# Optimization experiments

Measured on AMD Instinct MI355X. Metric: run time of the kernel, lower is better.

Reference implementation:

```python
import jax, jax.numpy as jnp
import numpy as np

N = 200000   # nodes
E = 600000   # directed edges
G = 8192     # graphs in batch
D_IN = 30
H = 128


def setup_inputs() -> dict:
    key = jax.random.key(0)
    ks = jax.random.split(key, 9)
    x = jax.random.normal(ks[0], (N, D_IN), jnp.float32)
    edge_index = jax.random.randint(ks[1], (2, E), 0, N, dtype=jnp.int32)
    batch_idx = jnp.sort(jax.random.randint(ks[2], (N,), 0, G, dtype=jnp.int32))
    W1 = jax.random.normal(ks[3], (D_IN, H), jnp.float32) / np.sqrt(D_IN)
    b1 = jnp.zeros((H,), jnp.float32)
    W2 = jax.random.normal(ks[4], (H, H), jnp.float32) / np.sqrt(H)
    b2 = jnp.zeros((H,), jnp.float32)
    W3 = jax.random.normal(ks[5], (H, H), jnp.float32) / np.sqrt(H)
    b3 = jnp.zeros((H,), jnp.float32)
    return {"x": x, "edge_index": edge_index, "batch_idx": batch_idx,
            "W1": W1, "b1": b1, "W2": W2, "b2": b2, "W3": W3, "b3": b3}


def _gcn_layer(x, W, b, src, dst, dinv):
    h = x @ W                                   # [N, H]
    norm = (dinv[src] * dinv[dst])[:, None]     # per-edge normalization
    msg = h[src] * norm                         # [E, H] gather + scale
    agg = jax.ops.segment_sum(msg, dst, num_segments=N)
    agg = agg + h * (dinv * dinv)[:, None]      # self-loop term, norm = 1/deg
    return jax.nn.relu(agg + b)


def reference(x, edge_index, batch_idx, W1, b1, W2, b2, W3, b3):
    src, dst = edge_index[0], edge_index[1]
    # degree with self-loops (edge weight 1), aggregated at target (col)
    deg = 1.0 + jax.ops.segment_sum(jnp.ones((E,), x.dtype), dst, num_segments=N)
    dinv = jax.lax.rsqrt(deg)                   # deg >= 1, safe
    h = _gcn_layer(x, W1, b1, src, dst, dinv)
    h = _gcn_layer(h, W2, b2, src, dst, dinv)
    h = _gcn_layer(h, W3, b3, src, dst, dinv)
    # global mean pool over batch segments
    sums = jax.ops.segment_sum(h, batch_idx, num_segments=G)
    counts = jax.ops.segment_sum(jnp.ones((N,), h.dtype), batch_idx, num_segments=G)
    return sums / jnp.maximum(counts, 1.0)[:, None]
```

## Files before the change

kernel.cpp:

```cpp
#include <hip/hip_runtime.h>


#define DIN 30
#define HD  128

typedef __attribute__((ext_vector_type(8))) short v8s;
typedef __attribute__((ext_vector_type(4))) float v4f;

static __device__ __forceinline__ unsigned short f2bf(float f) {
  unsigned int u = __float_as_uint(f);
  u += 0x7fffu + ((u >> 16) & 1u);
  return (unsigned short)(u >> 16);
}
static __device__ __forceinline__ float bf2f(unsigned short s) {
  return __uint_as_float(((unsigned int)s) << 16);
}
static __device__ __forceinline__ float bflo(unsigned int u) {
  return __uint_as_float(u << 16);
}
static __device__ __forceinline__ float bfhi(unsigned int u) {
  return __uint_as_float(u & 0xffff0000u);
}

#define ACC8(v, s)                                            \
  {                                                           \
    a0 += (s) * (float)((v).x & 0xffu);                       \
    a1 += (s) * (float)(((v).x >> 8) & 0xffu);                \
    a2 += (s) * (float)(((v).x >> 16) & 0xffu);               \
    a3 += (s) * (float)((v).x >> 24);                         \
    a4 += (s) * (float)((v).y & 0xffu);                       \
    a5 += (s) * (float)(((v).y >> 8) & 0xffu);                \
    a6 += (s) * (float)(((v).y >> 16) & 0xffu);               \
    a7 += (s) * (float)((v).y >> 24);                         \
  }

__global__ void k_degree(const int* __restrict__ dst, int* __restrict__ deg,
                         int* __restrict__ eord, int E) {
  int e = blockIdx.x * blockDim.x + threadIdx.x;
  if (e < E) eord[e] = atomicAdd(&deg[dst[e]], 1);
}

__global__ void k_scan(const int* __restrict__ deg, int* __restrict__ scanbuf,
                       int* __restrict__ rowptr, float* __restrict__ dinv, int N) {
  __shared__ int s[256];
  __shared__ int sbase;
  int bid = blockIdx.x, tid = threadIdx.x;
  int base = bid * 1024 + tid * 4;
  int v[4]; int t = 0;
#pragma unroll
  for (int j = 0; j < 4; ++j) { int idx = base + j; v[j] = (idx < N) ? deg[idx] : 0; t += v[j]; }
  s[tid] = t; __syncthreads();
  for (int d = 1; d < 256; d <<= 1) {
    int u = (tid >= d) ? s[tid - d] : 0;
    __syncthreads();
    s[tid] += u;
    __syncthreads();
  }
  int myexcl = s[tid] - t;
  int blocktotal = s[255];
  if (tid == 0) atomicExch(&scanbuf[bid], blocktotal | 0x80000000);

  int pre = 0;
  for (int p = tid; p < bid; p += 256) {
    int val;
    do { val = atomicAdd(&scanbuf[p], 0); } while (!(val & 0x80000000));
    pre += val & 0x7fffffff;
  }
  __syncthreads();
  s[tid] = pre; __syncthreads();
  for (int d = 128; d > 0; d >>= 1) { if (tid < d) s[tid] += s[tid + d]; __syncthreads(); }
  if (tid == 0) sbase = s[0];
  __syncthreads();

  int run = sbase + myexcl;
#pragma unroll
  for (int j = 0; j < 4; ++j) {
    int idx = base + j;
    if (idx < N) {
      rowptr[idx] = run;
      dinv[idx] = rsqrtf((float)(1 + v[j]));
    }
    run += v[j];
    if (idx == N - 1) rowptr[N] = run;
  }
}

static __device__ __forceinline__ void wtf_one(const float* __restrict__ W,
                                               unsigned short* __restrict__ WTF,
                                               int idx, int Kreal, int KK) {
  int j = idx & 7;
  int c = idx >> 3;
  int l15 = c & 15;
  int quad = (c >> 4) & 3;
  int kk = (c >> 6) % KK;
  int t = c / (64 * KK);
  int k = kk * 32 + quad * 8 + j;
  int n = t * 16 + l15;
  WTF[idx] = (k < Kreal) ? f2bf(W[k * 128 + n]) : (unsigned short)0;
}

__global__ void k_prep(const int* __restrict__ src, const int* __restrict__ dst,
                       const int* __restrict__ rowptr, const int* __restrict__ eord,
                       int* __restrict__ col, int E,
                       const float* __restrict__ x, const float* __restrict__ dinv,
                       unsigned short* __restrict__ xb, int N,
                       const float* __restrict__ W1, const float* __restrict__ W2,
                       const float* __restrict__ W3,
                       unsigned short* __restrict__ W1F, unsigned short* __restrict__ W2F,
                       unsigned short* __restrict__ W3F,
                       const int* __restrict__ batch, int* __restrict__ gstart, int G,
                       float* __restrict__ out,
                       int SB, int XB, int WB, int BB) {
  int blk = blockIdx.x;
  if (blk < SB) {
    int e = blk * 256 + threadIdx.x;
    if (e < E) col[rowptr[dst[e]] + eord[e]] = src[e];
  } else if (blk < SB + XB) {
    int idx = (blk - SB) * 256 + threadIdx.x;
    if (idx < N * 32) {
      int n = idx >> 5, f = idx & 31;
      float v = (f < DIN) ? x[(size_t)n * DIN + f] * dinv[n] : 0.f;
      xb[idx] = f2bf(v);
    }
  } else if (blk < SB + XB + WB) {
    int idx = (blk - SB - XB) * 256 + threadIdx.x;
    if (idx < 4096) wtf_one(W1, W1F, idx, DIN, 1);
    else if (idx < 20480) wtf_one(W2, W2F, idx - 4096, 128, 4);
    else if (idx < 36864) wtf_one(W3, W3F, idx - 20480, 128, 4);
  } else if (blk < SB + XB + WB + BB) {
    int i = (blk - SB - XB - WB) * 256 + threadIdx.x;
    if (i >= N) return;
    int b = batch[i];
    int prev = (i == 0) ? -1 : batch[i - 1];
    for (int g = prev + 1; g <= b; ++g) gstart[g] = i;
    if (i == N - 1)
      for (int g = b + 1; g <= G; ++g) gstart[g] = N;
  } else {
    int idx = (blk - SB - XB - WB - BB) * 256 + threadIdx.x;
    if (idx < G * 32)
      ((float4*)out)[idx] = make_float4(0.f, 0.f, 0.f, 0.f);
  }
}

template <int K>
__global__ __launch_bounds__(1024, 8) void k_fused(const void* __restrict__ hin,
                                                   const float* __restrict__ hscale,
                                                   const unsigned short* __restrict__ WTF,
                                                   const float* __restrict__ b,
                                                   const int* __restrict__ rowptr,
                                                   const int* __restrict__ col,
                                                   const float* __restrict__ dinv,
                                                   unsigned char* __restrict__ Cq,
                                                   float* __restrict__ Cs, int N) {
  constexpr int KK = K / 32;
  constexpr int KP = (K == 128) ? 136 : 40;
  constexpr int CP = 132;
  constexpr int SMSZ = (64 * KP > 64 * CP) ? 64 * KP : 64 * CP;
  constexpr int CH = 256;
  constexpr int SST = (K == 128) ? 144 : 72;
  __shared__ __align__(16) unsigned short sm[SMSZ];
  __shared__ __align__(16) unsigned char stg[CH * SST];
  __shared__ float sscale[(K == 128) ? CH : 1];

  int tid = threadIdx.x;
  int l16 = tid & 15;
  int g = tid >> 4;
  int row0 = blockIdx.x * 64;
  int node = row0 + g;
  int rend = row0 + 64; if (rend > N) rend = N;

  float a0 = 0.f, a1 = 0.f, a2 = 0.f, a3 = 0.f, a4 = 0.f, a5 = 0.f, a6 = 0.f, a7 = 0.f;
  int e0 = 0, e1 = 0; float di = 0.f;
  if (node < N) {
    e0 = rowptr[node]; e1 = rowptr[node + 1]; di = dinv[node];
    if constexpr (K == 32) {
      unsigned int u = ((const unsigned int*)hin)[(size_t)node * 16 + l16];
      a0 = bflo(u); a1 = bfhi(u);
    } else {
      uint2 u = ((const uint2*)hin)[(size_t)node * 16 + l16];
      float s = hscale[node];
      ACC8(u, s);
    }
  }
  int eb = rowptr[row0];
  int ee = rowptr[rend];

  for (int c0 = eb; c0 < ee; c0 += CH) {
#pragma unroll
    for (int q = 0; q < (CH * 8) / 1024; ++q) {
      int slot = q * 1024 + tid;
      int eL = slot >> 3, l8 = slot & 7;
      int e = c0 + eL;
      if (e < ee) {
        int c = col[e];
        if constexpr (K == 32) {
          uint2 v = ((const uint2*)hin)[(size_t)c * 8 + l8];
          *(uint2*)&stg[eL * SST + l8 * 8] = v;
        } else {
          uint4 v = ((const uint4*)hin)[(size_t)c * 8 + l8];
          *(uint4*)&stg[eL * SST + l8 * 16] = v;
          if (l8 == 0) sscale[eL] = hscale[c];
        }
      }
    }
    __syncthreads();
    int lo = (e0 > c0) ? e0 : c0;
    int hi = (e1 < c0 + CH) ? e1 : (c0 + CH);
    int e2 = lo;
    for (; e2 + 2 <= hi; e2 += 2) {
      int i0 = e2 - c0, i1 = i0 + 1;
      if constexpr (K == 32) {
        unsigned int w0 = *(const unsigned int*)&stg[i0 * SST + l16 * 4];
        unsigned int w1 = *(const unsigned int*)&stg[i1 * SST + l16 * 4];
        a0 += bflo(w0); a1 += bfhi(w0);
        a0 += bflo(w1); a1 += bfhi(w1);
      } else {
        uint2 w0 = *(const uint2*)&stg[i0 * SST + l16 * 8];
        uint2 w1 = *(const uint2*)&stg[i1 * SST + l16 * 8];
        float s0 = sscale[i0], s1 = sscale[i1];
        ACC8(w0, s0);
        ACC8(w1, s1);
      }
    }
    if (e2 < hi) {
      int i0 = e2 - c0;
      if constexpr (K == 32) {
        unsigned int w0 = *(const unsigned int*)&stg[i0 * SST + l16 * 4];
        a0 += bflo(w0); a1 += bfhi(w0);
      } else {
        uint2 w0 = *(const uint2*)&stg[i0 * SST + l16 * 8];
        float s0 = sscale[i0];
        ACC8(w0, s0);
      }
    }
    __syncthreads();
  }

  if constexpr (K == 32) {
    *(unsigned int*)&sm[g * KP + l16 * 2] =
        (unsigned int)f2bf(a0 * di) | ((unsigned int)f2bf(a1 * di) << 16);
  } else {
    uint4 o;
    o.x = (unsigned int)f2bf(a0 * di) | ((unsigned int)f2bf(a1 * di) << 16);
    o.y = (unsigned int)f2bf(a2 * di) | ((unsigned int)f2bf(a3 * di) << 16);
    o.z = (unsigned int)f2bf(a4 * di) | ((unsigned int)f2bf(a5 * di) << 16);
    o.w = (unsigned int)f2bf(a6 * di) | ((unsigned int)f2bf(a7 * di) << 16);
    *(uint4*)&sm[g * KP + l16 * 8] = o;
  }
  __syncthreads();

  int wv = tid >> 6, lane = tid & 63, quad = lane >> 4, l15 = lane & 15;
  int rt = wv & 3, tp = wv >> 2;
  v8s af[KK];
#pragma unroll
  for (int kk = 0; kk < KK; ++kk)
    af[kk] = *(const v8s*)&sm[(rt * 16 + l15) * KP + kk * 32 + quad * 8];
  __syncthreads();

  int crow0 = row0 + rt * 16 + quad * 4;
  float dr[4];
  if (crow0 + 3 < N) {
    float4 d4 = *(const float4*)&dinv[crow0];
    dr[0] = d4.x; dr[1] = d4.y; dr[2] = d4.z; dr[3] = d4.w;
  } else {
#pragma unroll
    for (int i = 0; i < 4; ++i) dr[i] = (crow0 + i < N) ? dinv[crow0 + i] : 0.f;
  }

#pragma unroll
  for (int tt = 0; tt < 2; ++tt) {
    int t = tp * 2 + tt;
    v4f acc = {0.f, 0.f, 0.f, 0.f};
#pragma unroll
    for (int kk = 0; kk < KK; ++kk) {
      v8s bf = *(const v8s*)(WTF + (size_t)(((t * KK + kk) * 4 + quad) * 16 + l15) * 8);
      acc = __builtin_amdgcn_mfma_f32_16x16x32_bf16(af[kk], bf, acc, 0, 0, 0);
    }
    float bias = b[t * 16 + l15];
#pragma unroll
    for (int i = 0; i < 4; ++i) {
      float o = fmaxf(acc[i] + bias, 0.f) * dr[i];
      sm[(rt * 16 + quad * 4 + i) * CP + t * 16 + l15] = f2bf(o);
    }
  }
  __syncthreads();

  {
    uint4 u = *(const uint4*)&sm[g * CP + l16 * 8];
    float f0 = bflo(u.x), f1 = bfhi(u.x), f2 = bflo(u.y), f3 = bfhi(u.y);
    float f4 = bflo(u.z), f5 = bfhi(u.z), f6 = bflo(u.w), f7 = bfhi(u.w);
    float m = fmaxf(fmaxf(fmaxf(f0, f1), fmaxf(f2, f3)),
                    fmaxf(fmaxf(f4, f5), fmaxf(f6, f7)));
    m = fmaxf(m, __shfl_xor(m, 1));
    m = fmaxf(m, __shfl_xor(m, 2));
    m = fmaxf(m, __shfl_xor(m, 4));
    m = fmaxf(m, __shfl_xor(m, 8));
    float inv = (m > 0.f) ? 255.f / m : 0.f;
    unsigned q0 = (unsigned)__float2int_rn(fminf(f0 * inv, 255.f));
    unsigned q1 = (unsigned)__float2int_rn(fminf(f1 * inv, 255.f));
    unsigned q2 = (unsigned)__float2int_rn(fminf(f2 * inv, 255.f));
    unsigned q3 = (unsigned)__float2int_rn(fminf(f3 * inv, 255.f));
    unsigned q4 = (unsigned)__float2int_rn(fminf(f4 * inv, 255.f));
    unsigned q5 = (unsigned)__float2int_rn(fminf(f5 * inv, 255.f));
    unsigned q6 = (unsigned)__float2int_rn(fminf(f6 * inv, 255.f));
    unsigned q7 = (unsigned)__float2int_rn(fminf(f7 * inv, 255.f));
    uint2 o;
    o.x = q0 | (q1 << 8) | (q2 << 16) | (q3 << 24);
    o.y = q4 | (q5 << 8) | (q6 << 16) | (q7 << 24);
    int row = row0 + g;
    if (row < N) {
      ((uint2*)Cq)[(size_t)row * 16 + l16] = o;
      if (l16 == 0) Cs[row] = m * (1.f / 255.f);
    }
  }
}

__global__ __launch_bounds__(1024, 8) void k_fused_pool(const unsigned char* __restrict__ hin,
                                                        const float* __restrict__ hscale,
                                                        const unsigned short* __restrict__ WTF,
                                                        const float* __restrict__ b,
                                                        const int* __restrict__ rowptr,
                                                        const int* __restrict__ col,
                                                        const float* __restrict__ dinv,
                                                        const int* __restrict__ batch,
                                                        float* __restrict__ out, int N) {
  constexpr int KK = 4, KP = 136, CP = 132;
  constexpr int SMSZ = 64 * KP;
  constexpr int CH = 256, SST = 144;
  __shared__ __align__(16) unsigned short sm[SMSZ];
  __shared__ __align__(16) unsigned char stg[CH * SST];
  __shared__ float sscale[CH];
  __shared__ int sbatch[64];

  int tid = threadIdx.x;
  int l16 = tid & 15;
  int g = tid >> 4;
  int row0 = blockIdx.x * 64;
  int node = row0 + g;
  int rend = row0 + 64; if (rend > N) rend = N;

  if (tid < 64) sbatch[tid] = (row0 + tid < N) ? batch[row0 + tid] : -1;

  float a0 = 0.f, a1 = 0.f, a2 = 0.f, a3 = 0.f, a4 = 0.f, a5 = 0.f, a6 = 0.f, a7 = 0.f;
  int e0 = 0, e1 = 0; float di = 0.f;
  if (node < N) {
    e0 = rowptr[node]; e1 = rowptr[node + 1]; di = dinv[node];
    uint2 u = ((const uint2*)hin)[(size_t)node * 16 + l16];
    float s = hscale[node];
    ACC8(u, s);
  }
  int eb = rowptr[row0];
  int ee = rowptr[rend];

  for (int c0 = eb; c0 < ee; c0 += CH) {
#pragma unroll
    for (int q = 0; q < 2; ++q) {
      int slot = q * 1024 + tid;
      int eL = slot >> 3, l8 = slot & 7;
      int e = c0 + eL;
      if (e < ee) {
        int c = col[e];
        uint4 v = ((const uint4*)hin)[(size_t)c * 8 + l8];
        *(uint4*)&stg[eL * SST + l8 * 16] = v;
        if (l8 == 0) sscale[eL] = hscale[c];
      }
    }
    __syncthreads();
    int lo = (e0 > c0) ? e0 : c0;
    int hi = (e1 < c0 + CH) ? e1 : (c0 + CH);
    int e2 = lo;
    for (; e2 + 2 <= hi; e2 += 2) {
      int i0 = e2 - c0, i1 = i0 + 1;
      uint2 w0 = *(const uint2*)&stg[i0 * SST + l16 * 8];
      uint2 w1 = *(const uint2*)&stg[i1 * SST + l16 * 8];
      float s0 = sscale[i0], s1 = sscale[i1];
      ACC8(w0, s0);
      ACC8(w1, s1);
    }
    if (e2 < hi) {
      int i0 = e2 - c0;
      uint2 w0 = *(const uint2*)&stg[i0 * SST + l16 * 8];
      float s0 = sscale[i0];
      ACC8(w0, s0);
    }
    __syncthreads();
  }

  {
    uint4 o;
    o.x = (unsigned int)f2bf(a0 * di) | ((unsigned int)f2bf(a1 * di) << 16);
    o.y = (unsigned int)f2bf(a2 * di) | ((unsigned int)f2bf(a3 * di) << 16);
    o.z = (unsigned int)f2bf(a4 * di) | ((unsigned int)f2bf(a5 * di) << 16);
    o.w = (unsigned int)f2bf(a6 * di) | ((unsigned int)f2bf(a7 * di) << 16);
    *(uint4*)&sm[g * KP + l16 * 8] = o;
  }
  __syncthreads();

  int wv = tid >> 6, lane = tid & 63, quad = lane >> 4, l15 = lane & 15;
  int rt = wv & 3, tp = wv >> 2;
  v8s af[KK];
#pragma unroll
  for (int kk = 0; kk < KK; ++kk)
    af[kk] = *(const v8s*)&sm[(rt * 16 + l15) * KP + kk * 32 + quad * 8];
  __syncthreads();

#pragma unroll
  for (int tt = 0; tt < 2; ++tt) {
    int t = tp * 2 + tt;
    v4f acc = {0.f, 0.f, 0.f, 0.f};
#pragma unroll
    for (int kk = 0; kk < KK; ++kk) {
      v8s bf = *(const v8s*)(WTF + (size_t)(((t * KK + kk) * 4 + quad) * 16 + l15) * 8);
      acc = __builtin_amdgcn_mfma_f32_16x16x32_bf16(af[kk], bf, acc, 0, 0, 0);
    }
    float bias = b[t * 16 + l15];
#pragma unroll
    for (int i = 0; i < 4; ++i) {
      float o = fmaxf(acc[i] + bias, 0.f);
      sm[(rt * 16 + quad * 4 + i) * CP + t * 16 + l15] = f2bf(o);
    }
  }
  __syncthreads();

  int f = tid & 127;
  int grp = tid >> 7;
  float run = 0.f;
  int cur = -1;
#pragma unroll
  for (int j = 0; j < 8; ++j) {
    int r = grp * 8 + j;
    int gg = sbatch[r];
    if (gg != cur) {
      if (cur >= 0) atomicAdd(&out[(size_t)cur * 128 + f], run);
      run = 0.f; cur = gg;
    }
    if (gg >= 0) run += bf2f(sm[r * CP + f]);
  }
  if (cur >= 0) atomicAdd(&out[(size_t)cur * 128 + f], run);
}

__global__ void k_finalize(float* __restrict__ out, const int* __restrict__ gstart, int G) {
  int idx = blockIdx.x * blockDim.x + threadIdx.x;
  if (idx >= G * 128) return;
  int g = idx >> 7;
  float cnt = (float)(gstart[g + 1] - gstart[g]);
  out[idx] = out[idx] / fmaxf(cnt, 1.f);
}

extern "C" void kernel_launch(void* const* d_in, const int* in_sizes, int n_in,
                              void* d_out, int out_size, void* d_ws, size_t ws_size,
                              hipStream_t stream) {
  const float* x  = (const float*)d_in[0];
  const int* ei   = (const int*)d_in[1];
  const int* batch = (const int*)d_in[2];
  const float* W1 = (const float*)d_in[3];
  const float* b1 = (const float*)d_in[4];
  const float* W2 = (const float*)d_in[5];
  const float* b2 = (const float*)d_in[6];
  const float* W3 = (const float*)d_in[7];
  const float* b3 = (const float*)d_in[8];
  float* out = (float*)d_out;
  int N = in_sizes[2];
  int E = in_sizes[1] / 2;
  int G = out_size / HD;
  const int* src = ei;
  const int* dst = ei + E;

  size_t off = 0;
  char* ws = (char*)d_ws;
  auto alloc = [&](size_t bytes) -> void* {
    void* p = ws + off;
    off += (bytes + 255) & ~(size_t)255;
    return p;
  };
  int nb1024 = (N + 1023) / 1024;
  int*   deg     = (int*)alloc((size_t)N * 4);
  int*   scanbuf = (int*)alloc((size_t)nb1024 * 4);
  float* dinv    = (float*)alloc((size_t)N * 4);
  int*   rowptr  = (int*)alloc((size_t)(N + 1) * 4);
  int*   eord    = (int*)alloc((size_t)E * 4);
  int*   col     = (int*)alloc((size_t)E * 4);
  int*   gstart  = (int*)alloc((size_t)(G + 1) * 4);
  unsigned short* xb  = (unsigned short*)alloc((size_t)N * 32 * 2);
  unsigned char*  hAq = (unsigned char*)alloc((size_t)N * 128);
  float*          hAs = (float*)alloc((size_t)N * 4);
  unsigned char*  hBq = (unsigned char*)alloc((size_t)N * 128);
  float*          hBs = (float*)alloc((size_t)N * 4);
  unsigned short* W1F = (unsigned short*)alloc(4096 * 2);
  unsigned short* W2F = (unsigned short*)alloc(16384 * 2);
  unsigned short* W3F = (unsigned short*)alloc(16384 * 2);
  (void)ws_size; (void)n_in;

  size_t zbytes = (size_t)((char*)dinv - (char*)deg);
  hipMemsetAsync(deg, 0, zbytes, stream);
  k_degree<<<(E + 255) / 256, 256, 0, stream>>>(dst, deg, eord, E);
  k_scan<<<nb1024, 256, 0, stream>>>(deg, scanbuf, rowptr, dinv, N);

  int SB = (E + 255) / 256;
  int XB = (N * 32 + 255) / 256;
  int WB = 144;
  int BB = (N + 255) / 256;
  int ZB = (G * 32 + 255) / 256;
  k_prep<<<SB + XB + WB + BB + ZB, 256, 0, stream>>>(src, dst, rowptr, eord, col, E,
                                                     x, dinv, xb, N,
                                                     W1, W2, W3, W1F, W2F, W3F,
                                                     batch, gstart, G, out,
                                                     SB, XB, WB, BB);

  int fusedBlocks = (N + 63) / 64;
  k_fused<32><<<fusedBlocks, 1024, 0, stream>>>(xb, nullptr, W1F, b1, rowptr, col, dinv,
                                                hAq, hAs, N);
  k_fused<128><<<fusedBlocks, 1024, 0, stream>>>(hAq, hAs, W2F, b2, rowptr, col, dinv,
                                                 hBq, hBs, N);
  k_fused_pool<<<fusedBlocks, 1024, 0, stream>>>(hBq, hBs, W3F, b3, rowptr, col, dinv,
                                                 batch, out, N);
  k_finalize<<<(G * 128 + 255) / 256, 256, 0, stream>>>(out, gstart, G);
}
```

Baseline: 286.0 us.

## Materialize per-edge messages via source-sorted gather before each fused layer

Builds a source-sorted edge list with a permutation into destination order, then adds a separate gather kernel per layer that reads node features in source order and scatters them into a dense per-edge message buffer laid out in destination (CSR) order. The fused aggregation kernels then stream contiguous messages instead of doing random indexed reads through col. The aim is more coalesced, cache-friendly feature reads. The cost is an extra E x 128-byte buffer written and read per layer, a second degree count, a second scan, and extra kernel launches.

New measurement: 371.3 us. 29.8% more time.

```diff
diff --git a/kernel.cpp b/kernel.cpp
--- a/kernel.cpp
+++ b/kernel.cpp
@@ -34,21 +34,25 @@
     a7 += (s) * (float)((v).y >> 24);                         \
   }
 
-__global__ void k_degree(const int* __restrict__ dst, int* __restrict__ deg,
-                         int* __restrict__ eord, int E) {
+__global__ void k_degree2(const int* __restrict__ src, const int* __restrict__ dst,
+                          int* __restrict__ deg, int* __restrict__ sdeg,
+                          int* __restrict__ eord, int* __restrict__ seord, int E) {
   int e = blockIdx.x * blockDim.x + threadIdx.x;
-  if (e < E) eord[e] = atomicAdd(&deg[dst[e]], 1);
-}
-
-__global__ void k_scan(const int* __restrict__ deg, int* __restrict__ scanbuf,
-                       int* __restrict__ rowptr, float* __restrict__ dinv, int N) {
+  if (e < E) {
+    eord[e] = atomicAdd(&deg[dst[e]], 1);
+    seord[e] = atomicAdd(&sdeg[src[e]], 1);
+  }
+}
+
+__global__ void k_scan(const int* __restrict__ cnt, int* __restrict__ scanbuf,
+                       int* __restrict__ outptr, float* __restrict__ dinvp, int N) {
   __shared__ int s[256];
   __shared__ int sbase;
   int bid = blockIdx.x, tid = threadIdx.x;
   int base = bid * 1024 + tid * 4;
   int v[4]; int t = 0;
 #pragma unroll
-  for (int j = 0; j < 4; ++j) { int idx = base + j; v[j] = (idx < N) ? deg[idx] : 0; t += v[j]; }
+  for (int j = 0; j < 4; ++j) { int idx = base + j; v[j] = (idx < N) ? cnt[idx] : 0; t += v[j]; }
   s[tid] = t; __syncthreads();
   for (int d = 1; d < 256; d <<= 1) {
     int u = (tid >= d) ? s[tid - d] : 0;
@@ -77,11 +81,11 @@
   for (int j = 0; j < 4; ++j) {
     int idx = base + j;
     if (idx < N) {
-      rowptr[idx] = run;
-      dinv[idx] = rsqrtf((float)(1 + v[j]));
+      outptr[idx] = run;
+      if (dinvp) dinvp[idx] = rsqrtf((float)(1 + v[j]));
     }
     run += v[j];
-    if (idx == N - 1) rowptr[N] = run;
+    if (idx == N - 1) outptr[N] = run;
   }
 }
 
@@ -100,8 +104,9 @@
 }
 
 __global__ void k_prep(const int* __restrict__ src, const int* __restrict__ dst,
-                       const int* __restrict__ rowptr, const int* __restrict__ eord,
-                       int* __restrict__ col, int E,
+                       const int* __restrict__ rowptr, const int* __restrict__ srowptr,
+                       const int* __restrict__ eord, const int* __restrict__ seord,
+                       int* __restrict__ ssrc, int* __restrict__ sperm, int E,
                        const float* __restrict__ x, const float* __restrict__ dinv,
                        unsigned short* __restrict__ xb, int N,
                        const float* __restrict__ W1, const float* __restrict__ W2,
@@ -114,7 +119,13 @@
   int blk = blockIdx.x;
   if (blk < SB) {
     int e = blk * 256 + threadIdx.x;
-    if (e < E) col[rowptr[dst[e]] + eord[e]] = src[e];
+    if (e < E) {
+      int d = dst[e], s = src[e];
+      int pos_d = rowptr[d] + eord[e];
+      int pos_s = srowptr[s] + seord[e];
+      ssrc[pos_s] = s;
+      sperm[pos_s] = pos_d;
+    }
   } else if (blk < SB + XB) {
     int idx = (blk - SB) * 256 + threadIdx.x;
     if (idx < N * 32) {
@@ -142,13 +153,32 @@
   }
 }
 
+template <int RB>
+__global__ void k_gather(const void* __restrict__ hin, const float* __restrict__ hs,
+                         const int* __restrict__ ssrc, const int* __restrict__ sperm,
+                         void* __restrict__ msg, float* __restrict__ mscale, int E) {
+  constexpr int L = RB / 16;
+  int idx = blockIdx.x * blockDim.x + threadIdx.x;
+  int e = idx / L;
+  int l = idx & (L - 1);
+  if (e >= E) return;
+  int s = ssrc[e];
+  int p = sperm[e];
+  uint4 v = ((const uint4*)hin)[(size_t)s * L + l];
+  ((uint4*)msg)[(size_t)p * L + l] = v;
+  if constexpr (RB == 128) {
+    if (l == 0) mscale[p] = hs[s];
+  }
+}
+
 template <int K>
 __global__ __launch_bounds__(1024, 8) void k_fused(const void* __restrict__ hin,
                                                    const float* __restrict__ hscale,
+                                                   const void* __restrict__ msg,
+                                                   const float* __restrict__ mscale,
                                                    const unsigned short* __restrict__ WTF,
                                                    const float* __restrict__ b,
                                                    const int* __restrict__ rowptr,
-                                                   const int* __restrict__ col,
                                                    const float* __restrict__ dinv,
                                                    unsigned char* __restrict__ Cq,
                                                    float* __restrict__ Cs, int N) {
@@ -187,19 +217,18 @@
 
   for (int c0 = eb; c0 < ee; c0 += CH) {
 #pragma unroll
-    for (int q = 0; q < (CH * 8) / 1024; ++q) {
+    for (int q = 0; q < 2; ++q) {
       int slot = q * 1024 + tid;
       int eL = slot >> 3, l8 = slot & 7;
       int e = c0 + eL;
       if (e < ee) {
-        int c = col[e];
         if constexpr (K == 32) {
-          uint2 v = ((const uint2*)hin)[(size_t)c * 8 + l8];
+          uint2 v = ((const uint2*)msg)[(size_t)e * 8 + l8];
           *(uint2*)&stg[eL * SST + l8 * 8] = v;
         } else {
-          uint4 v = ((const uint4*)hin)[(size_t)c * 8 + l8];
+          uint4 v = ((const uint4*)msg)[(size_t)e * 8 + l8];
           *(uint4*)&stg[eL * SST + l8 * 16] = v;
-          if (l8 == 0) sscale[eL] = hscale[c];
+          if (l8 == 0) sscale[eL] = mscale[e];
         }
       }
     }
@@ -317,10 +346,11 @@
 
 __global__ __launch_bounds__(1024, 8) void k_fused_pool(const unsigned char* __restrict__ hin,
                                                         const float* __restrict__ hscale,
+                                                        const void* __restrict__ msg,
+                                                        const float* __restrict__ mscale,
                                                         const unsigned short* __restrict__ WTF,
                                                         const float* __restrict__ b,
                                                         const int* __restrict__ rowptr,
-                                                        const int* __restrict__ col,
                                                         const float* __restrict__ dinv,
                                                         const int* __restrict__ batch,
                                                         float* __restrict__ out, int N) {
@@ -359,10 +389,9 @@
       int eL = slot >> 3, l8 = slot & 7;
       int e = c0 + eL;
       if (e < ee) {
-        int c = col[e];
-        uint4 v = ((const uint4*)hin)[(size_t)c * 8 + l8];
+        uint4 v = ((const uint4*)msg)[(size_t)e * 8 + l8];
         *(uint4*)&stg[eL * SST + l8 * 16] = v;
-        if (l8 == 0) sscale[eL] = hscale[c];
+        if (l8 == 0) sscale[eL] = mscale[e];
       }
     }
     __syncthreads();
@@ -474,18 +503,25 @@
     return p;
   };
   int nb1024 = (N + 1023) / 1024;
-  int*   deg     = (int*)alloc((size_t)N * 4);
-  int*   scanbuf = (int*)alloc((size_t)nb1024 * 4);
+  int*   deg      = (int*)alloc((size_t)N * 4);
+  int*   sdeg     = (int*)alloc((size_t)N * 4);
+  int*   scanbuf  = (int*)alloc((size_t)nb1024 * 4);
+  int*   scanbuf2 = (int*)alloc((size_t)nb1024 * 4);
   float* dinv    = (float*)alloc((size_t)N * 4);
   int*   rowptr  = (int*)alloc((size_t)(N + 1) * 4);
+  int*   srowptr = (int*)alloc((size_t)(N + 1) * 4);
   int*   eord    = (int*)alloc((size_t)E * 4);
-  int*   col     = (int*)alloc((size_t)E * 4);
+  int*   seord   = (int*)alloc((size_t)E * 4);
+  int*   ssrc    = (int*)alloc((size_t)E * 4);
+  int*   sperm   = (int*)alloc((size_t)E * 4);
   int*   gstart  = (int*)alloc((size_t)(G + 1) * 4);
   unsigned short* xb  = (unsigned short*)alloc((size_t)N * 32 * 2);
   unsigned char*  hAq = (unsigned char*)alloc((size_t)N * 128);
   float*          hAs = (float*)alloc((size_t)N * 4);
   unsigned char*  hBq = (unsigned char*)alloc((size_t)N * 128);
   float*          hBs = (float*)alloc((size_t)N * 4);
+  unsigned char*  msg = (unsigned char*)alloc((size_t)E * 128);
+  float*          mscale = (float*)alloc((size_t)E * 4);
   unsigned short* W1F = (unsigned short*)alloc(4096 * 2);
   unsigned short* W2F = (unsigned short*)alloc(16384 * 2);
   unsigned short* W3F = (unsigned short*)alloc(16384 * 2);
@@ -493,26 +529,34 @@
 
   size_t zbytes = (size_t)((char*)dinv - (char*)deg);
   hipMemsetAsync(deg, 0, zbytes, stream);
-  k_degree<<<(E + 255) / 256, 256, 0, stream>>>(dst, deg, eord, E);
+  k_degree2<<<(E + 255) / 256, 256, 0, stream>>>(src, dst, deg, sdeg, eord, seord, E);
   k_scan<<<nb1024, 256, 0, stream>>>(deg, scanbuf, rowptr, dinv, N);
+  k_scan<<<nb1024, 256, 0, stream>>>(sdeg, scanbuf2, srowptr, nullptr, N);
 
   int SB = (E + 255) / 256;
   int XB = (N * 32 + 255) / 256;
   int WB = 144;
   int BB = (N + 255) / 256;
   int ZB = (G * 32 + 255) / 256;
-  k_prep<<<SB + XB + WB + BB + ZB, 256, 0, stream>>>(src, dst, rowptr, eord, col, E,
+  k_prep<<<SB + XB + WB + BB + ZB, 256, 0, stream>>>(src, dst, rowptr, srowptr,
+                                                     eord, seord, ssrc, sperm, E,
                                                      x, dinv, xb, N,
                                                      W1, W2, W3, W1F, W2F, W3F,
                                                      batch, gstart, G, out,
                                                      SB, XB, WB, BB);
 
   int fusedBlocks = (N + 63) / 64;
-  k_fused<32><<<fusedBlocks, 1024, 0, stream>>>(xb, nullptr, W1F, b1, rowptr, col, dinv,
-                                                hAq, hAs, N);
-  k_fused<128><<<fusedBlocks, 1024, 0, stream>>>(hAq, hAs, W2F, b2, rowptr, col, dinv,
-                                                 hBq, hBs, N);
-  k_fused_pool<<<fusedBlocks, 1024, 0, stream>>>(hBq, hBs, W3F, b3, rowptr, col, dinv,
-                                                 batch, out, N);
+  k_gather<64><<<(E * 4 + 255) / 256, 256, 0, stream>>>(xb, nullptr, ssrc, sperm,
+                                                        msg, nullptr, E);
+  k_fused<32><<<fusedBlocks, 1024, 0, stream>>>(xb, nullptr, msg, nullptr,
+                                                W1F, b1, rowptr, dinv, hAq, hAs, N);
+  k_gather<128><<<(E * 8 + 255) / 256, 256, 0, stream>>>(hAq, hAs, ssrc, sperm,
+                                                         msg, mscale, E);
+  k_fused<128><<<fusedBlocks, 1024, 0, stream>>>(hAq, hAs, msg, mscale,
+                                                 W2F, b2, rowptr, dinv, hBq, hBs, N);
+  k_gather<128><<<(E * 8 + 255) / 256, 256, 0, stream>>>(hBq, hBs, ssrc, sperm,
+                                                         msg, mscale, E);
+  k_fused_pool<<<fusedBlocks, 1024, 0, stream>>>(hBq, hBs, msg, mscale,
+                                                 W3F, b3, rowptr, dinv, batch, out, N);
   k_finalize<<<(G * 128 + 255) / 256, 256, 0, stream>>>(out, gstart, G);
 }
```

## Store hidden activations as bf16 and gather neighbor rows via direct global-to-LDS loads

Applied to the files above, without the earlier changes.

Hidden activations between layers change from per-row-scaled uint8 to bf16, so the per-row max/quantize step and the per-edge scale multiply go away. The neighbor gather now stages column indices in shared memory and uses global_load_lds to copy rows straight into LDS, bypassing registers. The edge chunk size for the 128-wide layers is halved to keep LDS use bounded. The cost is twice the gather and store traffic per row and an extra barrier per chunk.

Result: faster. 278.6 us (-2.6%).

```diff
diff --git a/kernel.cpp b/kernel.cpp
--- a/kernel.cpp
+++ b/kernel.cpp
@@ -22,16 +22,18 @@
   return __uint_as_float(u & 0xffff0000u);
 }
 
-#define ACC8(v, s)                                            \
-  {                                                           \
-    a0 += (s) * (float)((v).x & 0xffu);                       \
-    a1 += (s) * (float)(((v).x >> 8) & 0xffu);                \
-    a2 += (s) * (float)(((v).x >> 16) & 0xffu);               \
-    a3 += (s) * (float)((v).x >> 24);                         \
-    a4 += (s) * (float)((v).y & 0xffu);                       \
-    a5 += (s) * (float)(((v).y >> 8) & 0xffu);                \
-    a6 += (s) * (float)(((v).y >> 16) & 0xffu);               \
-    a7 += (s) * (float)((v).y >> 24);                         \
+static __device__ __forceinline__ void gload_lds16(const void* g, void* l) {
+  __builtin_amdgcn_global_load_lds(
+      (const __attribute__((address_space(1))) void*)g,
+      (__attribute__((address_space(3))) void*)l, 16, 0, 0);
+}
+
+#define ADD8(v)                          \
+  {                                      \
+    a0 += bflo((v).x); a1 += bfhi((v).x); \
+    a2 += bflo((v).y); a3 += bfhi((v).y); \
+    a4 += bflo((v).z); a5 += bfhi((v).z); \
+    a6 += bflo((v).w); a7 += bfhi((v).w); \
   }
 
 __global__ void k_degree(const int* __restrict__ dst, int* __restrict__ deg,
@@ -143,28 +145,27 @@
 }
 
 template <int K>
-__global__ __launch_bounds__(1024, 8) void k_fused(const void* __restrict__ hin,
-                                                   const float* __restrict__ hscale,
+__global__ __launch_bounds__(1024, 8) void k_fused(const unsigned short* __restrict__ hin,
                                                    const unsigned short* __restrict__ WTF,
                                                    const float* __restrict__ b,
                                                    const int* __restrict__ rowptr,
                                                    const int* __restrict__ col,
                                                    const float* __restrict__ dinv,
-                                                   unsigned char* __restrict__ Cq,
-                                                   float* __restrict__ Cs, int N) {
+                                                   unsigned short* __restrict__ C, int N) {
   constexpr int KK = K / 32;
   constexpr int KP = (K == 128) ? 136 : 40;
   constexpr int CP = 132;
   constexpr int SMSZ = (64 * KP > 64 * CP) ? 64 * KP : 64 * CP;
-  constexpr int CH = 256;
-  constexpr int SST = (K == 128) ? 144 : 72;
+  constexpr int CH = (K == 128) ? 128 : 256;
+  constexpr int RB = K * 2;
   __shared__ __align__(16) unsigned short sm[SMSZ];
-  __shared__ __align__(16) unsigned char stg[CH * SST];
-  __shared__ float sscale[(K == 128) ? CH : 1];
+  __shared__ __align__(16) unsigned char stg[CH * RB];
+  __shared__ int smcol[CH];
 
   int tid = threadIdx.x;
   int l16 = tid & 15;
   int g = tid >> 4;
+  int lane = tid & 63, wv = tid >> 6, quad = lane >> 4, l15 = lane & 15;
   int row0 = blockIdx.x * 64;
   int node = row0 + g;
   int rend = row0 + 64; if (rend > N) rend = N;
@@ -177,31 +178,32 @@
       unsigned int u = ((const unsigned int*)hin)[(size_t)node * 16 + l16];
       a0 = bflo(u); a1 = bfhi(u);
     } else {
-      uint2 u = ((const uint2*)hin)[(size_t)node * 16 + l16];
-      float s = hscale[node];
-      ACC8(u, s);
+      uint4 u = ((const uint4*)hin)[(size_t)node * 16 + l16];
+      ADD8(u);
     }
   }
   int eb = rowptr[row0];
   int ee = rowptr[rend];
 
   for (int c0 = eb; c0 < ee; c0 += CH) {
-#pragma unroll
-    for (int q = 0; q < (CH * 8) / 1024; ++q) {
-      int slot = q * 1024 + tid;
-      int eL = slot >> 3, l8 = slot & 7;
-      int e = c0 + eL;
-      if (e < ee) {
-        int c = col[e];
-        if constexpr (K == 32) {
-          uint2 v = ((const uint2*)hin)[(size_t)c * 8 + l8];
-          *(uint2*)&stg[eL * SST + l8 * 8] = v;
-        } else {
-          uint4 v = ((const uint4*)hin)[(size_t)c * 8 + l8];
-          *(uint4*)&stg[eL * SST + l8 * 16] = v;
-          if (l8 == 0) sscale[eL] = hscale[c];
-        }
+    if (tid < CH) {
+      int e = c0 + tid;
+      smcol[tid] = (e < ee) ? col[e] : 0;
+    }
+    __syncthreads();
+    if constexpr (K == 128) {
+#pragma unroll
+      for (int q = 0; q < 2; ++q) {
+        int slb = wv * 8 + q * 4;
+        int row = smcol[slb + (lane >> 4)];
+        const unsigned short* gp = hin + (size_t)row * 128 + (lane & 15) * 8;
+        gload_lds16(gp, &stg[slb * 256]);
       }
+    } else {
+      int slb = wv * 16;
+      int row = smcol[slb + (lane >> 2)];
+      const unsigned short* gp = hin + (size_t)row * 32 + (lane & 3) * 8;
+      gload_lds16(gp, &stg[slb * 64]);
     }
     __syncthreads();
     int lo = (e0 > c0) ? e0 : c0;
@@ -210,27 +212,25 @@
     for (; e2 + 2 <= hi; e2 += 2) {
       int i0 = e2 - c0, i1 = i0 + 1;
       if constexpr (K == 32) {
-        unsigned int w0 = *(const unsigned int*)&stg[i0 * SST + l16 * 4];
-        unsigned int w1 = *(const unsigned int*)&stg[i1 * SST + l16 * 4];
+        unsigned int w0 = *(const unsigned int*)&stg[i0 * 64 + l16 * 4];
+        unsigned int w1 = *(const unsigned int*)&stg[i1 * 64 + l16 * 4];
         a0 += bflo(w0); a1 += bfhi(w0);
         a0 += bflo(w1); a1 += bfhi(w1);
       } else {
-        uint2 w0 = *(const uint2*)&stg[i0 * SST + l16 * 8];
-        uint2 w1 = *(const uint2*)&stg[i1 * SST + l16 * 8];
-        float s0 = sscale[i0], s1 = sscale[i1];
-        ACC8(w0, s0);
-        ACC8(w1, s1);
+        uint4 w0 = *(const uint4*)&stg[i0 * 256 + l16 * 16];
+        uint4 w1 = *(const uint4*)&stg[i1 * 256 + l16 * 16];
+        ADD8(w0);
+        ADD8(w1);
       }
     }
     if (e2 < hi) {
       int i0 = e2 - c0;
       if constexpr (K == 32) {
-        unsigned int w0 = *(const unsigned int*)&stg[i0 * SST + l16 * 4];
+        unsigned int w0 = *(const unsigned int*)&stg[i0 * 64 + l16 * 4];
         a0 += bflo(w0); a1 += bfhi(w0);
       } else {
-        uint2 w0 = *(const uint2*)&stg[i0 * SST + l16 * 8];
-        float s0 = sscale[i0];
-        ACC8(w0, s0);
+        uint4 w0 = *(const uint4*)&stg[i0 * 256 + l16 * 16];
+        ADD8(w0);
       }
     }
     __syncthreads();
@@ -249,7 +249,6 @@
   }
   __syncthreads();
 
-  int wv = tid >> 6, lane = tid & 63, quad = lane >> 4, l15 = lane & 15;
   int rt = wv & 3, tp = wv >> 2;
   v8s af[KK];
 #pragma unroll
@@ -285,38 +284,17 @@
   }
   __syncthreads();
 
-  {
-    uint4 u = *(const uint4*)&sm[g * CP + l16 * 8];
-    float f0 = bflo(u.x), f1 = bfhi(u.x), f2 = bflo(u.y), f3 = bfhi(u.y);
-    float f4 = bflo(u.z), f5 = bfhi(u.z), f6 = bflo(u.w), f7 = bfhi(u.w);
-    float m = fmaxf(fmaxf(fmaxf(f0, f1), fmaxf(f2, f3)),
-                    fmaxf(fmaxf(f4, f5), fmaxf(f6, f7)));
-    m = fmaxf(m, __shfl_xor(m, 1));
-    m = fmaxf(m, __shfl_xor(m, 2));
-    m = fmaxf(m, __shfl_xor(m, 4));
-    m = fmaxf(m, __shfl_xor(m, 8));
-    float inv = (m > 0.f) ? 255.f / m : 0.f;
-    unsigned q0 = (unsigned)__float2int_rn(fminf(f0 * inv, 255.f));
-    unsigned q1 = (unsigned)__float2int_rn(fminf(f1 * inv, 255.f));
-    unsigned q2 = (unsigned)__float2int_rn(fminf(f2 * inv, 255.f));
-    unsigned q3 = (unsigned)__float2int_rn(fminf(f3 * inv, 255.f));
-    unsigned q4 = (unsigned)__float2int_rn(fminf(f4 * inv, 255.f));
-    unsigned q5 = (unsigned)__float2int_rn(fminf(f5 * inv, 255.f));
-    unsigned q6 = (unsigned)__float2int_rn(fminf(f6 * inv, 255.f));
-    unsigned q7 = (unsigned)__float2int_rn(fminf(f7 * inv, 255.f));
-    uint2 o;
-    o.x = q0 | (q1 << 8) | (q2 << 16) | (q3 << 24);
-    o.y = q4 | (q5 << 8) | (q6 << 16) | (q7 << 24);
-    int row = row0 + g;
-    if (row < N) {
-      ((uint2*)Cq)[(size_t)row * 16 + l16] = o;
-      if (l16 == 0) Cs[row] = m * (1.f / 255.f);
-    }
-  }
-}
-
-__global__ __launch_bounds__(1024, 8) void k_fused_pool(const unsigned char* __restrict__ hin,
-                                                        const float* __restrict__ hscale,
+#pragma unroll
+  for (int j = 0; j < 2; ++j) {
+    int linear = j * 1024 + tid;
+    int r = linear >> 5, ch = linear & 31;
+    uint2 v = *(const uint2*)&sm[r * CP + ch * 4];
+    int row = row0 + r;
+    if (row < N) ((uint2*)C)[(size_t)row * 32 + ch] = v;
+  }
+}
+
+__global__ __launch_bounds__(1024, 8) void k_fused_pool(const unsigned short* __restrict__ hin,
                                                         const unsigned short* __restrict__ WTF,
                                                         const float* __restrict__ b,
                                                         const int* __restrict__ rowptr,
@@ -326,15 +304,16 @@
                                                         float* __restrict__ out, int N) {
   constexpr int KK = 4, KP = 136, CP = 132;
   constexpr int SMSZ = 64 * KP;
-  constexpr int CH = 256, SST = 144;
+  constexpr int CH = 128;
   __shared__ __align__(16) unsigned short sm[SMSZ];
-  __shared__ __align__(16) unsigned char stg[CH * SST];
-  __shared__ float sscale[CH];
+  __shared__ __align__(16) unsigned char stg[CH * 256];
+  __shared__ int smcol[CH];
   __shared__ int sbatch[64];
 
   int tid = threadIdx.x;
   int l16 = tid & 15;
   int g = tid >> 4;
+  int lane = tid & 63, wv = tid >> 6, quad = lane >> 4, l15 = lane & 15;
   int row0 = blockIdx.x * 64;
   int node = row0 + g;
   int rend = row0 + 64; if (rend > N) rend = N;
@@ -345,25 +324,24 @@
   int e0 = 0, e1 = 0; float di = 0.f;
   if (node < N) {
     e0 = rowptr[node]; e1 = rowptr[node + 1]; di = dinv[node];
-    uint2 u = ((const uint2*)hin)[(size_t)node * 16 + l16];
-    float s = hscale[node];
-    ACC8(u, s);
+    uint4 u = ((const uint4*)hin)[(size_t)node * 16 + l16];
+    ADD8(u);
   }
   int eb = rowptr[row0];
   int ee = rowptr[rend];
 
   for (int c0 = eb; c0 < ee; c0 += CH) {
+    if (tid < CH) {
+      int e = c0 + tid;
+      smcol[tid] = (e < ee) ? col[e] : 0;
+    }
+    __syncthreads();
 #pragma unroll
     for (int q = 0; q < 2; ++q) {
-      int slot = q * 1024 + tid;
-      int eL = slot >> 3, l8 = slot & 7;
-      int e = c0 + eL;
-      if (e < ee) {
-        int c = col[e];
-        uint4 v = ((const uint4*)hin)[(size_t)c * 8 + l8];
-        *(uint4*)&stg[eL * SST + l8 * 16] = v;
-        if (l8 == 0) sscale[eL] = hscale[c];
-      }
+      int slb = wv * 8 + q * 4;
+      int row = smcol[slb + (lane >> 4)];
+      const unsigned short* gp = hin + (size_t)row * 128 + (lane & 15) * 8;
+      gload_lds16(gp, &stg[slb * 256]);
     }
     __syncthreads();
     int lo = (e0 > c0) ? e0 : c0;
@@ -371,17 +349,15 @@
     int e2 = lo;
     for (; e2 + 2 <= hi; e2 += 2) {
       int i0 = e2 - c0, i1 = i0 + 1;
-      uint2 w0 = *(const uint2*)&stg[i0 * SST + l16 * 8];
-      uint2 w1 = *(const uint2*)&stg[i1 * SST + l16 * 8];
-      float s0 = sscale[i0], s1 = sscale[i1];
-      ACC8(w0, s0);
-      ACC8(w1, s1);
+      uint4 w0 = *(const uint4*)&stg[i0 * 256 + l16 * 16];
+      uint4 w1 = *(const uint4*)&stg[i1 * 256 + l16 * 16];
+      ADD8(w0);
+      ADD8(w1);
     }
     if (e2 < hi) {
       int i0 = e2 - c0;
-      uint2 w0 = *(const uint2*)&stg[i0 * SST + l16 * 8];
-      float s0 = sscale[i0];
-      ACC8(w0, s0);
+      uint4 w0 = *(const uint4*)&stg[i0 * 256 + l16 * 16];
+      ADD8(w0);
     }
     __syncthreads();
   }
@@ -396,7 +372,6 @@
   }
   __syncthreads();
 
-  int wv = tid >> 6, lane = tid & 63, quad = lane >> 4, l15 = lane & 15;
   int rt = wv & 3, tp = wv >> 2;
   v8s af[KK];
 #pragma unroll
@@ -481,11 +456,9 @@
   int*   eord    = (int*)alloc((size_t)E * 4);
   int*   col     = (int*)alloc((size_t)E * 4);
   int*   gstart  = (int*)alloc((size_t)(G + 1) * 4);
-  unsigned short* xb  = (unsigned short*)alloc((size_t)N * 32 * 2);
-  unsigned char*  hAq = (unsigned char*)alloc((size_t)N * 128);
-  float*          hAs = (float*)alloc((size_t)N * 4);
-  unsigned char*  hBq = (unsigned char*)alloc((size_t)N * 128);
-  float*          hBs = (float*)alloc((size_t)N * 4);
+  unsigned short* xb = (unsigned short*)alloc((size_t)N * 32 * 2);
+  unsigned short* hA = (unsigned short*)alloc((size_t)N * HD * 2);
+  unsigned short* hB = (unsigned short*)alloc((size_t)N * HD * 2);
   unsigned short* W1F = (unsigned short*)alloc(4096 * 2);
   unsigned short* W2F = (unsigned short*)alloc(16384 * 2);
   unsigned short* W3F = (unsigned short*)alloc(16384 * 2);
@@ -508,11 +481,8 @@
                                                      SB, XB, WB, BB);
 
   int fusedBlocks = (N + 63) / 64;
-  k_fused<32><<<fusedBlocks, 1024, 0, stream>>>(xb, nullptr, W1F, b1, rowptr, col, dinv,
-                                                hAq, hAs, N);
-  k_fused<128><<<fusedBlocks, 1024, 0, stream>>>(hAq, hAs, W2F, b2, rowptr, col, dinv,
-                                                 hBq, hBs, N);
-  k_fused_pool<<<fusedBlocks, 1024, 0, stream>>>(hBq, hBs, W3F, b3, rowptr, col, dinv,
-                                                 batch, out, N);
+  k_fused<32><<<fusedBlocks, 1024, 0, stream>>>(xb, W1F, b1, rowptr, col, dinv, hA, N);
+  k_fused<128><<<fusedBlocks, 1024, 0, stream>>>(hA, W2F, b2, rowptr, col, dinv, hB, N);
+  k_fused_pool<<<fusedBlocks, 1024, 0, stream>>>(hB, W3F, b3, rowptr, col, dinv, batch, out, N);
   k_finalize<<<(G * 128 + 255) / 256, 256, 0, stream>>>(out, gstart, G);
 }
```

## Shrink fused GCN blocks to 16 rows and gather neighbours via global_load_lds

Applied to the files above, without the earlier changes.

The fused aggregate+GEMM kernels now use 256-thread blocks covering 16 nodes instead of 1024-thread blocks covering 64. Neighbour rows are staged with direct global-to-LDS loads driven by a column-index list cached in shared memory, rather than register-mediated loads followed by LDS stores. The x-to-bf16 prep also writes 16-byte vectors per thread instead of one element per thread. This aims to cut LDS footprint and per-block barrier stalls and to raise occupancy. In exchange it adds an extra barrier per chunk and removes the padded LDS row stride, which may cause bank conflicts.

New measurement: 237.5 us. -17.0%, faster.

```diff
diff --git a/kernel.cpp b/kernel.cpp
--- a/kernel.cpp
+++ b/kernel.cpp
@@ -20,6 +20,12 @@
 }
 static __device__ __forceinline__ float bfhi(unsigned int u) {
   return __uint_as_float(u & 0xffff0000u);
+}
+
+static __device__ __forceinline__ void gload_lds16(const void* g, void* l) {
+  __builtin_amdgcn_global_load_lds(
+      (const __attribute__((address_space(1))) void*)g,
+      (__attribute__((address_space(3))) void*)l, 16, 0, 0);
 }
 
 #define ACC8(v, s)                                            \
@@ -117,10 +123,19 @@
     if (e < E) col[rowptr[dst[e]] + eord[e]] = src[e];
   } else if (blk < SB + XB) {
     int idx = (blk - SB) * 256 + threadIdx.x;
-    if (idx < N * 32) {
-      int n = idx >> 5, f = idx & 31;
-      float v = (f < DIN) ? x[(size_t)n * DIN + f] * dinv[n] : 0.f;
-      xb[idx] = f2bf(v);
+    if (idx < N * 4) {
+      int n = idx >> 2, s4 = idx & 3, f0 = s4 * 8;
+      float di = dinv[n];
+      unsigned int w[4];
+#pragma unroll
+      for (int j = 0; j < 8; j += 2) {
+        int f = f0 + j;
+        float v0 = (f < DIN) ? x[(size_t)n * DIN + f] * di : 0.f;
+        float v1 = (f + 1 < DIN) ? x[(size_t)n * DIN + f + 1] * di : 0.f;
+        w[j >> 1] = (unsigned int)f2bf(v0) | ((unsigned int)f2bf(v1) << 16);
+      }
+      uint4 o; o.x = w[0]; o.y = w[1]; o.z = w[2]; o.w = w[3];
+      ((uint4*)xb)[idx] = o;
     }
   } else if (blk < SB + XB + WB) {
     int idx = (blk - SB - XB) * 256 + threadIdx.x;
@@ -143,31 +158,33 @@
 }
 
 template <int K>
-__global__ __launch_bounds__(1024, 8) void k_fused(const void* __restrict__ hin,
-                                                   const float* __restrict__ hscale,
-                                                   const unsigned short* __restrict__ WTF,
-                                                   const float* __restrict__ b,
-                                                   const int* __restrict__ rowptr,
-                                                   const int* __restrict__ col,
-                                                   const float* __restrict__ dinv,
-                                                   unsigned char* __restrict__ Cq,
-                                                   float* __restrict__ Cs, int N) {
+__global__ __launch_bounds__(256, 8) void k_fused(const void* __restrict__ hin,
+                                                  const float* __restrict__ hscale,
+                                                  const unsigned short* __restrict__ WTF,
+                                                  const float* __restrict__ b,
+                                                  const int* __restrict__ rowptr,
+                                                  const int* __restrict__ col,
+                                                  const float* __restrict__ dinv,
+                                                  unsigned char* __restrict__ Cq,
+                                                  float* __restrict__ Cs, int N) {
   constexpr int KK = K / 32;
   constexpr int KP = (K == 128) ? 136 : 40;
   constexpr int CP = 132;
-  constexpr int SMSZ = (64 * KP > 64 * CP) ? 64 * KP : 64 * CP;
-  constexpr int CH = 256;
-  constexpr int SST = (K == 128) ? 144 : 72;
+  constexpr int SMSZ = (16 * KP > 16 * CP) ? 16 * KP : 16 * CP;
+  constexpr int CH = 64;
+  constexpr int RB = (K == 128) ? 128 : 64;
   __shared__ __align__(16) unsigned short sm[SMSZ];
-  __shared__ __align__(16) unsigned char stg[CH * SST];
+  __shared__ __align__(16) unsigned char stg[CH * RB];
+  __shared__ int smcol[CH];
   __shared__ float sscale[(K == 128) ? CH : 1];
 
   int tid = threadIdx.x;
   int l16 = tid & 15;
   int g = tid >> 4;
-  int row0 = blockIdx.x * 64;
+  int lane = tid & 63, wv = tid >> 6, quad = lane >> 4, l15 = lane & 15;
+  int row0 = blockIdx.x * 16;
   int node = row0 + g;
-  int rend = row0 + 64; if (rend > N) rend = N;
+  int rend = row0 + 16; if (rend > N) rend = N;
 
   float a0 = 0.f, a1 = 0.f, a2 = 0.f, a3 = 0.f, a4 = 0.f, a5 = 0.f, a6 = 0.f, a7 = 0.f;
   int e0 = 0, e1 = 0; float di = 0.f;
@@ -186,22 +203,26 @@
   int ee = rowptr[rend];
 
   for (int c0 = eb; c0 < ee; c0 += CH) {
-#pragma unroll
-    for (int q = 0; q < (CH * 8) / 1024; ++q) {
-      int slot = q * 1024 + tid;
-      int eL = slot >> 3, l8 = slot & 7;
-      int e = c0 + eL;
-      if (e < ee) {
-        int c = col[e];
-        if constexpr (K == 32) {
-          uint2 v = ((const uint2*)hin)[(size_t)c * 8 + l8];
-          *(uint2*)&stg[eL * SST + l8 * 8] = v;
-        } else {
-          uint4 v = ((const uint4*)hin)[(size_t)c * 8 + l8];
-          *(uint4*)&stg[eL * SST + l8 * 16] = v;
-          if (l8 == 0) sscale[eL] = hscale[c];
-        }
+    if (tid < CH) {
+      int e = c0 + tid;
+      int c = (e < ee) ? col[e] : 0;
+      smcol[tid] = c;
+      if constexpr (K == 128) sscale[tid] = hscale[c];
+    }
+    __syncthreads();
+    if constexpr (K == 128) {
+#pragma unroll
+      for (int q = 0; q < 2; ++q) {
+        int slb = wv * 16 + q * 8;
+        int row = smcol[slb + (lane >> 3)];
+        const unsigned char* gp = (const unsigned char*)hin + (size_t)row * 128 + (lane & 7) * 16;
+        gload_lds16(gp, &stg[slb * 128]);
       }
+    } else {
+      int slb = wv * 16;
+      int row = smcol[slb + (lane >> 2)];
+      const unsigned short* gp = (const unsigned short*)hin + (size_t)row * 32 + (lane & 3) * 8;
+      gload_lds16(gp, &stg[slb * 64]);
     }
     __syncthreads();
     int lo = (e0 > c0) ? e0 : c0;
@@ -210,13 +231,13 @@
     for (; e2 + 2 <= hi; e2 += 2) {
       int i0 = e2 - c0, i1 = i0 + 1;
       if constexpr (K == 32) {
-        unsigned int w0 = *(const unsigned int*)&stg[i0 * SST + l16 * 4];
-        unsigned int w1 = *(const unsigned int*)&stg[i1 * SST + l16 * 4];
+        unsigned int w0 = *(const unsigned int*)&stg[i0 * 64 + l16 * 4];
+        unsigned int w1 = *(const unsigned int*)&stg[i1 * 64 + l16 * 4];
         a0 += bflo(w0); a1 += bfhi(w0);
         a0 += bflo(w1); a1 += bfhi(w1);
       } else {
-        uint2 w0 = *(const uint2*)&stg[i0 * SST + l16 * 8];
-        uint2 w1 = *(const uint2*)&stg[i1 * SST + l16 * 8];
+        uint2 w0 = *(const uint2*)&stg[i0 * 128 + l16 * 8];
+        uint2 w1 = *(const uint2*)&stg[i1 * 128 + l16 * 8];
         float s0 = sscale[i0], s1 = sscale[i1];
         ACC8(w0, s0);
         ACC8(w1, s1);
@@ -225,10 +246,10 @@
     if (e2 < hi) {
       int i0 = e2 - c0;
       if constexpr (K == 32) {
-        unsigned int w0 = *(const unsigned int*)&stg[i0 * SST + l16 * 4];
+        unsigned int w0 = *(const unsigned int*)&stg[i0 * 64 + l16 * 4];
         a0 += bflo(w0); a1 += bfhi(w0);
       } else {
-        uint2 w0 = *(const uint2*)&stg[i0 * SST + l16 * 8];
+        uint2 w0 = *(const uint2*)&stg[i0 * 128 + l16 * 8];
         float s0 = sscale[i0];
         ACC8(w0, s0);
       }
@@ -249,15 +270,13 @@
   }
   __syncthreads();
 
-  int wv = tid >> 6, lane = tid & 63, quad = lane >> 4, l15 = lane & 15;
-  int rt = wv & 3, tp = wv >> 2;
   v8s af[KK];
 #pragma unroll
   for (int kk = 0; kk < KK; ++kk)
-    af[kk] = *(const v8s*)&sm[(rt * 16 + l15) * KP + kk * 32 + quad * 8];
-  __syncthreads();
-
-  int crow0 = row0 + rt * 16 + quad * 4;
+    af[kk] = *(const v8s*)&sm[l15 * KP + kk * 32 + quad * 8];
+  __syncthreads();
+
+  int crow0 = row0 + quad * 4;
   float dr[4];
   if (crow0 + 3 < N) {
     float4 d4 = *(const float4*)&dinv[crow0];
@@ -269,7 +288,7 @@
 
 #pragma unroll
   for (int tt = 0; tt < 2; ++tt) {
-    int t = tp * 2 + tt;
+    int t = wv * 2 + tt;
     v4f acc = {0.f, 0.f, 0.f, 0.f};
 #pragma unroll
     for (int kk = 0; kk < KK; ++kk) {
@@ -280,7 +299,7 @@
 #pragma unroll
     for (int i = 0; i < 4; ++i) {
       float o = fmaxf(acc[i] + bias, 0.f) * dr[i];
-      sm[(rt * 16 + quad * 4 + i) * CP + t * 16 + l15] = f2bf(o);
+      sm[(quad * 4 + i) * CP + t * 16 + l15] = f2bf(o);
     }
   }
   __syncthreads();
@@ -315,31 +334,33 @@
   }
 }
 
-__global__ __launch_bounds__(1024, 8) void k_fused_pool(const unsigned char* __restrict__ hin,
-                                                        const float* __restrict__ hscale,
-                                                        const unsigned short* __restrict__ WTF,
-                                                        const float* __restrict__ b,
-                                                        const int* __restrict__ rowptr,
-                                                        const int* __restrict__ col,
-                                                        const float* __restrict__ dinv,
-                                                        const int* __restrict__ batch,
-                                                        float* __restrict__ out, int N) {
+__global__ __launch_bounds__(256, 8) void k_fused_pool(const unsigned char* __restrict__ hin,
+                                                       const float* __restrict__ hscale,
+                                                       const unsigned short* __restrict__ WTF,
+                                                       const float* __restrict__ b,
+                                                       const int* __restrict__ rowptr,
+                                                       const int* __restrict__ col,
+                                                       const float* __restrict__ dinv,
+                                                       const int* __restrict__ batch,
+                                                       float* __restrict__ out, int N) {
   constexpr int KK = 4, KP = 136, CP = 132;
-  constexpr int SMSZ = 64 * KP;
-  constexpr int CH = 256, SST = 144;
+  constexpr int SMSZ = 16 * KP;
+  constexpr int CH = 64;
   __shared__ __align__(16) unsigned short sm[SMSZ];
-  __shared__ __align__(16) unsigned char stg[CH * SST];
+  __shared__ __align__(16) unsigned char stg[CH * 128];
+  __shared__ int smcol[CH];
   __shared__ float sscale[CH];
-  __shared__ int sbatch[64];
+  __shared__ int sbatch[16];
 
   int tid = threadIdx.x;
   int l16 = tid & 15;
   int g = tid >> 4;
-  int row0 = blockIdx.x * 64;
+  int lane = tid & 63, wv = tid >> 6, quad = lane >> 4, l15 = lane & 15;
+  int row0 = blockIdx.x * 16;
   int node = row0 + g;
-  int rend = row0 + 64; if (rend > N) rend = N;
-
-  if (tid < 64) sbatch[tid] = (row0 + tid < N) ? batch[row0 + tid] : -1;
+  int rend = row0 + 16; if (rend > N) rend = N;
+
+  if (tid < 16) sbatch[tid] = (row0 + tid < N) ? batch[row0 + tid] : -1;
 
   float a0 = 0.f, a1 = 0.f, a2 = 0.f, a3 = 0.f, a4 = 0.f, a5 = 0.f, a6 = 0.f, a7 = 0.f;
   int e0 = 0, e1 = 0; float di = 0.f;
@@ -353,17 +374,19 @@
   int ee = rowptr[rend];
 
   for (int c0 = eb; c0 < ee; c0 += CH) {
+    if (tid < CH) {
+      int e = c0 + tid;
+      int c = (e < ee) ? col[e] : 0;
+      smcol[tid] = c;
+      sscale[tid] = hscale[c];
+    }
+    __syncthreads();
 #pragma unroll
     for (int q = 0; q < 2; ++q) {
-      int slot = q * 1024 + tid;
-      int eL = slot >> 3, l8 = slot & 7;
-      int e = c0 + eL;
-      if (e < ee) {
-        int c = col[e];
-        uint4 v = ((const uint4*)hin)[(size_t)c * 8 + l8];
-        *(uint4*)&stg[eL * SST + l8 * 16] = v;
-        if (l8 == 0) sscale[eL] = hscale[c];
-      }
+      int slb = wv * 16 + q * 8;
+      int row = smcol[slb + (lane >> 3)];
+      const unsigned char* gp = hin + (size_t)row * 128 + (lane & 7) * 16;
+      gload_lds16(gp, &stg[slb * 128]);
     }
     __syncthreads();
     int lo = (e0 > c0) ? e0 : c0;
@@ -371,15 +394,15 @@
     int e2 = lo;
     for (; e2 + 2 <= hi; e2 += 2) {
       int i0 = e2 - c0, i1 = i0 + 1;
-      uint2 w0 = *(const uint2*)&stg[i0 * SST + l16 * 8];
-      uint2 w1 = *(const uint2*)&stg[i1 * SST + l16 * 8];
+      uint2 w0 = *(const uint2*)&stg[i0 * 128 + l16 * 8];
+      uint2 w1 = *(const uint2*)&stg[i1 * 128 + l16 * 8];
       float s0 = sscale[i0], s1 = sscale[i1];
       ACC8(w0, s0);
       ACC8(w1, s1);
     }
     if (e2 < hi) {
       int i0 = e2 - c0;
-      uint2 w0 = *(const uint2*)&stg[i0 * SST + l16 * 8];
+      uint2 w0 = *(const uint2*)&stg[i0 * 128 + l16 * 8];
       float s0 = sscale[i0];
       ACC8(w0, s0);
     }
@@ -396,17 +419,15 @@
   }
   __syncthreads();
 
-  int wv = tid >> 6, lane = tid & 63, quad = lane >> 4, l15 = lane & 15;
-  int rt = wv & 3, tp = wv >> 2;
   v8s af[KK];
 #pragma unroll
   for (int kk = 0; kk < KK; ++kk)
-    af[kk] = *(const v8s*)&sm[(rt * 16 + l15) * KP + kk * 32 + quad * 8];
+    af[kk] = *(const v8s*)&sm[l15 * KP + kk * 32 + quad * 8];
   __syncthreads();
 
 #pragma unroll
   for (int tt = 0; tt < 2; ++tt) {
-    int t = tp * 2 + tt;
+    int t = wv * 2 + tt;
     v4f acc = {0.f, 0.f, 0.f, 0.f};
 #pragma unroll
     for (int kk = 0; kk < KK; ++kk) {
@@ -417,7 +438,7 @@
 #pragma unroll
     for (int i = 0; i < 4; ++i) {
       float o = fmaxf(acc[i] + bias, 0.f);
-      sm[(rt * 16 + quad * 4 + i) * CP + t * 16 + l15] = f2bf(o);
+      sm[(quad * 4 + i) * CP + t * 16 + l15] = f2bf(o);
     }
   }
   __syncthreads();
@@ -497,7 +518,7 @@
   k_scan<<<nb1024, 256, 0, stream>>>(deg, scanbuf, rowptr, dinv, N);
 
   int SB = (E + 255) / 256;
-  int XB = (N * 32 + 255) / 256;
+  int XB = (N * 4 + 255) / 256;
   int WB = 144;
   int BB = (N + 255) / 256;
   int ZB = (G * 32 + 255) / 256;
@@ -507,12 +528,12 @@
                                                      batch, gstart, G, out,
                                                      SB, XB, WB, BB);
 
-  int fusedBlocks = (N + 63) / 64;
-  k_fused<32><<<fusedBlocks, 1024, 0, stream>>>(xb, nullptr, W1F, b1, rowptr, col, dinv,
-                                                hAq, hAs, N);
-  k_fused<128><<<fusedBlocks, 1024, 0, stream>>>(hAq, hAs, W2F, b2, rowptr, col, dinv,
-                                                 hBq, hBs, N);
-  k_fused_pool<<<fusedBlocks, 1024, 0, stream>>>(hBq, hBs, W3F, b3, rowptr, col, dinv,
-                                                 batch, out, N);
+  int fusedBlocks = (N + 15) / 16;
+  k_fused<32><<<fusedBlocks, 256, 0, stream>>>(xb, nullptr, W1F, b1, rowptr, col, dinv,
+                                               hAq, hAs, N);
+  k_fused<128><<<fusedBlocks, 256, 0, stream>>>(hAq, hAs, W2F, b2, rowptr, col, dinv,
+                                                hBq, hBs, N);
+  k_fused_pool<<<fusedBlocks, 256, 0, stream>>>(hBq, hBs, W3F, b3, rowptr, col, dinv,
+                                                batch, out, N);
   k_finalize<<<(G * 128 + 255) / 256, 256, 0, stream>>>(out, gstart, G);
 }
```
